# Kernel tuning notes

Measured on AMD Instinct MI355X. Metric: run time of the kernel, lower is better.

## Reference

```python
import jax, jax.numpy as jnp
import numpy as np

CLAMP_MIN = 1e-12
CLAMP_MAX = 1e12


def setup_inputs() -> dict:
    key = jax.random.key(0)
    k1, k2, k3 = jax.random.split(key, 3)
    N, C, H, W = 32, 11, 384, 384
    x = jax.random.normal(k1, (N, C, H, W), dtype=jnp.float32)
    centers = jax.random.normal(k2, (N, C, H, W), dtype=jnp.float32)
    labels = jax.random.randint(k3, (N, H, W), 0, C, dtype=jnp.int64)
    return {"x": x, "centers": centers, "labels": labels}


def reference(x, centers, labels):
    # x, centers: (N, C, H, W); labels: (N, H, W) int
    N, C, H, W = x.shape
    # res[n,c] = x[n,c]^2 + centers[n,c]^2 - 2 * x[n,c] @ centers[n,c]
    # (single batched matmul replaces the original per-(i,j) addmm loop)
    res = x * x + centers * centers - 2.0 * jnp.matmul(x, centers)
    # softmax over class dim, then max over class dim -> (N, H, W)
    res_max = jnp.max(jax.nn.softmax(res, axis=1), axis=1)
    dist = res_max * labels.astype(res_max.dtype)
    loss = jnp.sum(jnp.clip(dist, CLAMP_MIN, CLAMP_MAX)) / (H * W * N)
    return loss
```

## Files before the change

kernel.cpp:

```cpp
#include <hip/hip_runtime.h>
#include <stdint.h>

typedef __attribute__((ext_vector_type(8))) short short8;
typedef __attribute__((ext_vector_type(4))) float floatx4;
typedef __attribute__((ext_vector_type(4))) unsigned short u16x4;

#define Hh 384
#define Ww 384
#define Cc 11
#define Nn 32
#define PITCH 72

__device__ __forceinline__ unsigned short f2bf(float f) {
  union { float f; uint32_t u; } z; z.f = f;
  return (unsigned short)(z.u >> 16);
}
__device__ __forceinline__ float bf2f(unsigned short b) {
  union { uint32_t u; float f; } z; z.u = ((uint32_t)b) << 16;
  return z.f;
}

__global__ __launch_bounds__(256, 4)
void center_loss(const float* __restrict__ X, const float* __restrict__ Cen,
                 const int* __restrict__ Lab, float* __restrict__ Out) {
  __shared__ __align__(16) unsigned short Alds[64 * PITCH];
  __shared__ __align__(16) unsigned short Blds[64 * PITCH];
  __shared__ float red[4];

  const int bx   = blockIdx.x;
  const int xcd  = bx & 7;
  const int slot = bx >> 3;
  const int grp  = slot / 36;
  const int t36  = slot - grp * 36;
  const int n    = xcd + (grp << 3);
  const int ib = t36 / 6;
  const int jb = t36 - ib * 6;
  const int i0 = ib << 6, j0 = jb << 6;

  const int t   = threadIdx.x;
  const int l   = t & 63;
  const int w   = t >> 6;
  const int wr  = (w >> 1) << 5;
  const int wc  = (w & 1) << 5;
  const int q4  = l >> 4;
  const int l16 = l & 15;
  const int sa  = t & 15;
  const int sr  = t >> 4;

  const size_t plane = (size_t)Hh * Ww;
  const float* xbase = X   + (size_t)n * Cc * plane;
  const float* cbase = Cen + (size_t)n * Cc * plane;

  float m[16], s[16];
#pragma unroll
  for (int i = 0; i < 16; ++i) { m[i] = -3.0e38f; s[i] = 0.0f; }

  floatx4 acc[2][2];
  float ev[16];
#pragma unroll
  for (int a = 0; a < 2; ++a)
#pragma unroll
    for (int b = 0; b < 2; ++b) acc[a][b] = (floatx4){0.f, 0.f, 0.f, 0.f};
#pragma unroll
  for (int i = 0; i < 16; ++i) ev[i] = 0.0f;

  float4 pa[4];
  float  pb[16];

  {
    const float* ap = xbase + (size_t)(i0 + sr) * Ww + (sa << 2);
#pragma unroll
    for (int p = 0; p < 4; ++p)
      pa[p] = *reinterpret_cast<const float4*>(ap + (size_t)(p * 16) * Ww);
#pragma unroll
    for (int p = 0; p < 2; ++p) {
      const int kbase = (w << 3) + (p << 5);
      const float* bp = cbase + (size_t)kbase * Ww + j0 + l;
#pragma unroll
      for (int u = 0; u < 8; ++u) pb[p * 8 + u] = bp[(size_t)u * Ww];
    }
  }

  int c = 0, kb = 0;
  for (int it = 0; it < 66; ++it) {
    __syncthreads();

#pragma unroll
    for (int p = 0; p < 4; ++p) {
      u16x4 pk;
      pk.x = f2bf(pa[p].x); pk.y = f2bf(pa[p].y);
      pk.z = f2bf(pa[p].z); pk.w = f2bf(pa[p].w);
      *reinterpret_cast<u16x4*>(&Alds[(sr + 16 * p) * PITCH + (sa << 2)]) = pk;
    }
#pragma unroll
    for (int p = 0; p < 2; ++p) {
      const int kbase = (w << 3) + (p << 5);
      short8 pk;
#pragma unroll
      for (int u = 0; u < 8; ++u) pk[u] = (short)f2bf(pb[p * 8 + u]);
      *reinterpret_cast<short8*>(&Blds[l * PITCH + kbase]) = pk;
    }

    int kn = kb + 1, cn = c;
    if (kn == 6) { kn = 0; cn = c + 1; }
    float4 na[4];
    float  nb[16];
    if (it < 65) {
      const float* xb = xbase + (size_t)cn * plane;
      const float* cb = cbase + (size_t)cn * plane;
      const float* ap = xb + (size_t)(i0 + sr) * Ww + (kn << 6) + (sa << 2);
#pragma unroll
      for (int p = 0; p < 4; ++p)
        na[p] = *reinterpret_cast<const float4*>(ap + (size_t)(p * 16) * Ww);
#pragma unroll
      for (int p = 0; p < 2; ++p) {
        const int kbase = (w << 3) + (p << 5);
        const float* bp = cb + (size_t)((kn << 6) + kbase) * Ww + j0 + l;
#pragma unroll
        for (int u = 0; u < 8; ++u) nb[p * 8 + u] = bp[(size_t)u * Ww];
      }
    }

    __syncthreads();

    if (kb == jb) {
#pragma unroll
      for (int fr = 0; fr < 2; ++fr)
#pragma unroll
        for (int fc = 0; fc < 2; ++fc)
#pragma unroll
          for (int r = 0; r < 4; ++r) {
            const int idx = ((fr << 1) + fc) * 4 + r;
            const int pr = wr + (fr << 4) + (q4 << 2) + r;
            const int pc = wc + (fc << 4) + l16;
            float xv = bf2f(Alds[pr * PITCH + pc]);
            ev[idx] += xv * xv;
          }
    }
    if (kb == ib) {
#pragma unroll
      for (int fr = 0; fr < 2; ++fr)
#pragma unroll
        for (int fc = 0; fc < 2; ++fc)
#pragma unroll
          for (int r = 0; r < 4; ++r) {
            const int idx = ((fr << 1) + fc) * 4 + r;
            const int pr = wr + (fr << 4) + (q4 << 2) + r;
            const int pc = wc + (fc << 4) + l16;
            float cv = bf2f(Blds[pc * PITCH + pr]);
            ev[idx] += cv * cv;
          }
    }

#pragma unroll
    for (int ks = 0; ks < 2; ++ks) {
      const int ko = (ks << 5) + (q4 << 3);
      short8 a0 = *reinterpret_cast<const short8*>(&Alds[(wr +      l16) * PITCH + ko]);
      short8 a1 = *reinterpret_cast<const short8*>(&Alds[(wr + 16 + l16) * PITCH + ko]);
      short8 b0 = *reinterpret_cast<const short8*>(&Blds[(wc +      l16) * PITCH + ko]);
      short8 b1 = *reinterpret_cast<const short8*>(&Blds[(wc + 16 + l16) * PITCH + ko]);
      acc[0][0] = __builtin_amdgcn_mfma_f32_16x16x32_bf16(a0, b0, acc[0][0], 0, 0, 0);
      acc[0][1] = __builtin_amdgcn_mfma_f32_16x16x32_bf16(a0, b1, acc[0][1], 0, 0, 0);
      acc[1][0] = __builtin_amdgcn_mfma_f32_16x16x32_bf16(a1, b0, acc[1][0], 0, 0, 0);
      acc[1][1] = __builtin_amdgcn_mfma_f32_16x16x32_bf16(a1, b1, acc[1][1], 0, 0, 0);
    }

    if (kb == 5) {
#pragma unroll
      for (int fr = 0; fr < 2; ++fr)
#pragma unroll
        for (int fc = 0; fc < 2; ++fc)
#pragma unroll
          for (int r = 0; r < 4; ++r) {
            const int idx = ((fr << 1) + fc) * 4 + r;
            float res = ev[idx] - 2.0f * acc[fr][fc][r];
            float mi = m[idx];
            if (res <= mi) {
              s[idx] += __expf(res - mi);
            } else {
              s[idx] = s[idx] * __expf(mi - res) + 1.0f;
              m[idx] = res;
            }
            acc[fr][fc][r] = 0.0f;
            ev[idx] = 0.0f;
          }
    }

    kb = kn; c = cn;
#pragma unroll
    for (int p = 0; p < 4; ++p) pa[p] = na[p];
#pragma unroll
    for (int p = 0; p < 16; ++p) pb[p] = nb[p];
  }

  float local = 0.0f;
  const int* lb = Lab + (size_t)n * plane;
#pragma unroll
  for (int fr = 0; fr < 2; ++fr)
#pragma unroll
    for (int fc = 0; fc < 2; ++fc)
#pragma unroll
      for (int r = 0; r < 4; ++r) {
        const int idx = ((fr << 1) + fc) * 4 + r;
        const int pr = i0 + wr + (fr << 4) + (q4 << 2) + r;
        const int pc = j0 + wc + (fc << 4) + l16;
        float val = 1.0f / s[idx];
        float d = val * (float)lb[pr * Ww + pc];
        d = fminf(fmaxf(d, 1e-12f), 1e12f);
        local += d;
      }
#pragma unroll
  for (int off = 32; off > 0; off >>= 1) local += __shfl_down(local, off, 64);
  if (l == 0) red[w] = local;
  __syncthreads();
  if (t == 0) {
    float bs = (red[0] + red[1] + red[2] + red[3]) * (1.0f / 4718592.0f);
    atomicAdd(Out, bs);
  }
}

extern "C" void kernel_launch(void* const* d_in, const int* in_sizes, int n_in,
                              void* d_out, int out_size, void* d_ws, size_t ws_size,
                              hipStream_t stream) {
  const float* X   = (const float*)d_in[0];
  const float* Cen = (const float*)d_in[1];
  const int*   Lab = (const int*)d_in[2];
  float* Out = (float*)d_out;
  hipMemsetAsync(Out, 0, (size_t)out_size * sizeof(float), stream);
  hipLaunchKernelGGL(center_loss, dim3(Nn * 36), dim3(256), 0, stream,
                     X, Cen, Lab, Out);
}
```

Baseline: 494.7 us.

## Shrink output tile to 64x32 with two-wave blocks and twice the grid

Splits each 64x64 output tile into two 64x32 tiles handled by 128-thread blocks, which doubles the grid to 2304 blocks. The global loads and LDS staging of A and B, the diagonal squared-term extraction, and the epilogue indexing are remapped to match. The intent is better occupancy and load balance across CUs, and less LDS per block. The cost is that each A tile of x is now loaded and converted twice, which increases global traffic for the A operand.

After: 675.4 us. 36.5% more time.

```diff
diff --git a/kernel.cpp b/kernel.cpp
--- a/kernel.cpp
+++ b/kernel.cpp
@@ -20,28 +20,27 @@
   return z.f;
 }
 
-__global__ __launch_bounds__(256, 4)
+__global__ __launch_bounds__(128, 4)
 void center_loss(const float* __restrict__ X, const float* __restrict__ Cen,
                  const int* __restrict__ Lab, float* __restrict__ Out) {
   __shared__ __align__(16) unsigned short Alds[64 * PITCH];
-  __shared__ __align__(16) unsigned short Blds[64 * PITCH];
-  __shared__ float red[4];
+  __shared__ __align__(16) unsigned short Blds[32 * PITCH];
+  __shared__ float red[2];
 
   const int bx   = blockIdx.x;
   const int xcd  = bx & 7;
   const int slot = bx >> 3;
-  const int grp  = slot / 36;
-  const int t36  = slot - grp * 36;
+  const int grp  = slot / 72;
+  const int t72  = slot - grp * 72;
   const int n    = xcd + (grp << 3);
-  const int ib = t36 / 6;
-  const int jb = t36 - ib * 6;
-  const int i0 = ib << 6, j0 = jb << 6;
+  const int ib   = t72 / 12;
+  const int jb   = t72 - ib * 12;
+  const int i0 = ib << 6, j0 = jb << 5;
 
   const int t   = threadIdx.x;
   const int l   = t & 63;
   const int w   = t >> 6;
-  const int wr  = (w >> 1) << 5;
-  const int wc  = (w & 1) << 5;
+  const int wr  = w << 5;
   const int q4  = l >> 4;
   const int l16 = l & 15;
   const int sa  = t & 15;
@@ -64,21 +63,20 @@
 #pragma unroll
   for (int i = 0; i < 16; ++i) ev[i] = 0.0f;
 
-  float4 pa[4];
+  float4 pa[8];
   float  pb[16];
+
+  const int bj  = l & 31;
+  const int bk0 = (w << 5) + ((l >> 5) << 4);
 
   {
     const float* ap = xbase + (size_t)(i0 + sr) * Ww + (sa << 2);
 #pragma unroll
-    for (int p = 0; p < 4; ++p)
-      pa[p] = *reinterpret_cast<const float4*>(ap + (size_t)(p * 16) * Ww);
-#pragma unroll
-    for (int p = 0; p < 2; ++p) {
-      const int kbase = (w << 3) + (p << 5);
-      const float* bp = cbase + (size_t)kbase * Ww + j0 + l;
-#pragma unroll
-      for (int u = 0; u < 8; ++u) pb[p * 8 + u] = bp[(size_t)u * Ww];
-    }
+    for (int p = 0; p < 8; ++p)
+      pa[p] = *reinterpret_cast<const float4*>(ap + (size_t)(p * 8) * Ww);
+    const float* bp = cbase + (size_t)bk0 * Ww + j0 + bj;
+#pragma unroll
+    for (int p = 0; p < 16; ++p) pb[p] = bp[(size_t)p * Ww];
   }
 
   int c = 0, kb = 0;
@@ -86,44 +84,39 @@
     __syncthreads();
 
 #pragma unroll
-    for (int p = 0; p < 4; ++p) {
+    for (int p = 0; p < 8; ++p) {
       u16x4 pk;
       pk.x = f2bf(pa[p].x); pk.y = f2bf(pa[p].y);
       pk.z = f2bf(pa[p].z); pk.w = f2bf(pa[p].w);
-      *reinterpret_cast<u16x4*>(&Alds[(sr + 16 * p) * PITCH + (sa << 2)]) = pk;
-    }
-#pragma unroll
-    for (int p = 0; p < 2; ++p) {
-      const int kbase = (w << 3) + (p << 5);
-      short8 pk;
-#pragma unroll
-      for (int u = 0; u < 8; ++u) pk[u] = (short)f2bf(pb[p * 8 + u]);
-      *reinterpret_cast<short8*>(&Blds[l * PITCH + kbase]) = pk;
+      *reinterpret_cast<u16x4*>(&Alds[(sr + 8 * p) * PITCH + (sa << 2)]) = pk;
+    }
+#pragma unroll
+    for (int q = 0; q < 4; ++q) {
+      u16x4 pk;
+      pk.x = f2bf(pb[q * 4 + 0]); pk.y = f2bf(pb[q * 4 + 1]);
+      pk.z = f2bf(pb[q * 4 + 2]); pk.w = f2bf(pb[q * 4 + 3]);
+      *reinterpret_cast<u16x4*>(&Blds[bj * PITCH + bk0 + (q << 2)]) = pk;
     }
 
     int kn = kb + 1, cn = c;
     if (kn == 6) { kn = 0; cn = c + 1; }
-    float4 na[4];
+    float4 na[8];
     float  nb[16];
     if (it < 65) {
       const float* xb = xbase + (size_t)cn * plane;
       const float* cb = cbase + (size_t)cn * plane;
       const float* ap = xb + (size_t)(i0 + sr) * Ww + (kn << 6) + (sa << 2);
 #pragma unroll
-      for (int p = 0; p < 4; ++p)
-        na[p] = *reinterpret_cast<const float4*>(ap + (size_t)(p * 16) * Ww);
-#pragma unroll
-      for (int p = 0; p < 2; ++p) {
-        const int kbase = (w << 3) + (p << 5);
-        const float* bp = cb + (size_t)((kn << 6) + kbase) * Ww + j0 + l;
-#pragma unroll
-        for (int u = 0; u < 8; ++u) nb[p * 8 + u] = bp[(size_t)u * Ww];
-      }
+      for (int p = 0; p < 8; ++p)
+        na[p] = *reinterpret_cast<const float4*>(ap + (size_t)(p * 8) * Ww);
+      const float* bp = cb + (size_t)((kn << 6) + bk0) * Ww + j0 + bj;
+#pragma unroll
+      for (int p = 0; p < 16; ++p) nb[p] = bp[(size_t)p * Ww];
     }
 
     __syncthreads();
 
-    if (kb == jb) {
+    if (kb == (jb >> 1)) {
 #pragma unroll
       for (int fr = 0; fr < 2; ++fr)
 #pragma unroll
@@ -132,7 +125,7 @@
           for (int r = 0; r < 4; ++r) {
             const int idx = ((fr << 1) + fc) * 4 + r;
             const int pr = wr + (fr << 4) + (q4 << 2) + r;
-            const int pc = wc + (fc << 4) + l16;
+            const int pc = ((jb & 1) << 5) + (fc << 4) + l16;
             float xv = bf2f(Alds[pr * PITCH + pc]);
             ev[idx] += xv * xv;
           }
@@ -145,9 +138,9 @@
 #pragma unroll
           for (int r = 0; r < 4; ++r) {
             const int idx = ((fr << 1) + fc) * 4 + r;
-            const int pr = wr + (fr << 4) + (q4 << 2) + r;
-            const int pc = wc + (fc << 4) + l16;
-            float cv = bf2f(Blds[pc * PITCH + pr]);
+            const int kk = wr + (fr << 4) + (q4 << 2) + r;
+            const int jj = (fc << 4) + l16;
+            float cv = bf2f(Blds[jj * PITCH + kk]);
             ev[idx] += cv * cv;
           }
     }
@@ -157,8 +150,8 @@
       const int ko = (ks << 5) + (q4 << 3);
       short8 a0 = *reinterpret_cast<const short8*>(&Alds[(wr +      l16) * PITCH + ko]);
       short8 a1 = *reinterpret_cast<const short8*>(&Alds[(wr + 16 + l16) * PITCH + ko]);
-      short8 b0 = *reinterpret_cast<const short8*>(&Blds[(wc +      l16) * PITCH + ko]);
-      short8 b1 = *reinterpret_cast<const short8*>(&Blds[(wc + 16 + l16) * PITCH + ko]);
+      short8 b0 = *reinterpret_cast<const short8*>(&Blds[(     l16) * PITCH + ko]);
+      short8 b1 = *reinterpret_cast<const short8*>(&Blds[(16 + l16) * PITCH + ko]);
       acc[0][0] = __builtin_amdgcn_mfma_f32_16x16x32_bf16(a0, b0, acc[0][0], 0, 0, 0);
       acc[0][1] = __builtin_amdgcn_mfma_f32_16x16x32_bf16(a0, b1, acc[0][1], 0, 0, 0);
       acc[1][0] = __builtin_amdgcn_mfma_f32_16x16x32_bf16(a1, b0, acc[1][0], 0, 0, 0);
@@ -188,7 +181,7 @@
 
     kb = kn; c = cn;
 #pragma unroll
-    for (int p = 0; p < 4; ++p) pa[p] = na[p];
+    for (int p = 0; p < 8; ++p) pa[p] = na[p];
 #pragma unroll
     for (int p = 0; p < 16; ++p) pb[p] = nb[p];
   }
@@ -203,7 +196,7 @@
       for (int r = 0; r < 4; ++r) {
         const int idx = ((fr << 1) + fc) * 4 + r;
         const int pr = i0 + wr + (fr << 4) + (q4 << 2) + r;
-        const int pc = j0 + wc + (fc << 4) + l16;
+        const int pc = j0 + (fc << 4) + l16;
         float val = 1.0f / s[idx];
         float d = val * (float)lb[pr * Ww + pc];
         d = fminf(fmaxf(d, 1e-12f), 1e12f);
@@ -214,7 +207,7 @@
   if (l == 0) red[w] = local;
   __syncthreads();
   if (t == 0) {
-    float bs = (red[0] + red[1] + red[2] + red[3]) * (1.0f / 4718592.0f);
+    float bs = (red[0] + red[1]) * (1.0f / 4718592.0f);
     atomicAdd(Out, bs);
   }
 }
@@ -227,6 +220,6 @@
   const int*   Lab = (const int*)d_in[2];
   float* Out = (float*)d_out;
   hipMemsetAsync(Out, 0, (size_t)out_size * sizeof(float), stream);
-  hipLaunchKernelGGL(center_loss, dim3(Nn * 36), dim3(256), 0, stream,
+  hipLaunchKernelGGL(center_loss, dim3(Nn * 72), dim3(128), 0, stream,
                      X, Cen, Lab, Out);
 }
```
